# Kernel tuning notes

Hardware: AMD Instinct MI355X
Metric: run time of the kernel (lower is better)

## Reference

```python
import jax, jax.numpy as jnp
import numpy as np

B, T, D, H = 2, 2048, 1024, 16
HD = D // H  # head dim = 64


def setup_inputs() -> dict:
    key = jax.random.key(0)
    ks = jax.random.split(key, 8)
    scale = 0.02
    return {
        "query_states": jax.random.normal(ks[0], (B, T, D), jnp.float32),
        "key_states": jax.random.normal(ks[1], (B, T, D), jnp.float32),
        "query_mask": jnp.ones((B, T), jnp.float32),
        "key_mask": jnp.ones((B, T), jnp.float32),
        "Wq": jax.random.normal(ks[2], (D, D), jnp.float32) * scale,
        "bq": jnp.zeros((D,), jnp.float32),
        "Wk": jax.random.normal(ks[3], (D, D), jnp.float32) * scale,
        "bk": jnp.zeros((D,), jnp.float32),
        "Wv": jax.random.normal(ks[4], (D, D), jnp.float32) * scale,
        "bv": jnp.zeros((D,), jnp.float32),
        "mask_future": 1,
    }


def _split_heads(x):  # [B,T,D] -> [B,H,T,HD]
    return x.reshape(B, T, H, HD).transpose(0, 2, 1, 3)


def reference(query_states, key_states, query_mask, key_mask, Wq, bq, Wk, bk, Wv, bv, mask_future):
    q = _split_heads(query_states @ Wq.T + bq)
    k = _split_heads(key_states @ Wk.T + bk)
    v = _split_heads(key_states @ Wv.T + bv)
    # [B,H,T,T]
    scores = jnp.einsum("bhqd,bhkd->bhqk", q, k) / jnp.sqrt(jnp.float32(HD))
    scores = scores + (1.0 - key_mask)[:, None, None, :] * -10000.0
    if mask_future:
        causal = (1.0 - jnp.tril(jnp.ones((T, T), jnp.float32))) * -10000.0
        scores = scores + causal[None, None, :, :]
    probs = jax.nn.softmax(scores, axis=-1)
    probs = probs * query_mask[:, None, :, None]  # post-softmax query mask
    ctx = jnp.einsum("bhqk,bhkd->bhqd", probs, v)
    return ctx.transpose(0, 2, 1, 3).reshape(B, T, D)
```

## Files before the change

### kernel.cpp

```cpp
#include <hip/hip_runtime.h>
#include <hip/hip_bf16.h>
#include <stdint.h>

typedef __attribute__((ext_vector_type(8))) short short8;
typedef __attribute__((ext_vector_type(4))) short short4_t;
typedef __attribute__((ext_vector_type(4))) float f32x4;

#define B_ 2
#define T_ 2048
#define D_ 1024
#define H_ 16
#define HD_ 64
#define BT_ 4096
#define NKT64 32

#define QSCALE 0.1803368801111601f
#define PEN2 14426.950408889634f

__device__ __forceinline__ unsigned short f2bf(float f) {
    union { float f; uint32_t u; } v; v.f = f;
    uint32_t u = v.u;
    uint32_t r = (u + 0x7fffu + ((u >> 16) & 1u)) >> 16;
    return (unsigned short)r;
}

__device__ __forceinline__ uint32_t cvtpk(float a, float b) {
    union { __hip_bfloat162 h; uint32_t u; } cv;
    cv.h = __float22bfloat162_rn(make_float2(a, b));
    return cv.u;
}

__device__ __forceinline__ void gld16(const void* g, void* l) {
    __builtin_amdgcn_global_load_lds((const __attribute__((address_space(1))) void*)g,
                                     (__attribute__((address_space(3))) void*)l, 16, 0, 0);
}

__device__ __forceinline__ int swz(int x) { return x ^ (((x >> 7) & 7) << 4); }

__global__ __launch_bounds__(256) void cvt_all(const float* __restrict__ xq, unsigned short* __restrict__ dxq,
                                               const float* __restrict__ xk, unsigned short* __restrict__ dxk,
                                               const float* __restrict__ Wq, unsigned short* __restrict__ dwq,
                                               const float* __restrict__ Wk, unsigned short* __restrict__ dwk,
                                               const float* __restrict__ Wv, unsigned short* __restrict__ dwv,
                                               const float* __restrict__ kmask, float* __restrict__ kpen_g) {
    const int NX = BT_ * D_ / 8;
    const int NW = D_ * D_ / 8;
    const int NKP = B_ * T_ / 8;
    const int total = NX * 2 + NW * 3 + NKP;
    for (int i = blockIdx.x * 256 + threadIdx.x; i < total; i += gridDim.x * 256) {
        int j = i;
        const float* s;
        unsigned short* d;
        if (j < NX) { s = xq; d = dxq; }
        else if ((j -= NX) < NX) { s = xk; d = dxk; }
        else if ((j -= NX) < NW) { s = Wq; d = dwq; }
        else if ((j -= NW) < NW) { s = Wk; d = dwk; }
        else if ((j -= NW) < NW) { s = Wv; d = dwv; }
        else {
            j -= NW;
            const float4* mk = (const float4*)kmask + (size_t)j * 2;
            float4 a = mk[0], b4 = mk[1];
            float4 o0 = make_float4((1.0f - a.x) * -PEN2, (1.0f - a.y) * -PEN2,
                                    (1.0f - a.z) * -PEN2, (1.0f - a.w) * -PEN2);
            float4 o1 = make_float4((1.0f - b4.x) * -PEN2, (1.0f - b4.y) * -PEN2,
                                    (1.0f - b4.z) * -PEN2, (1.0f - b4.w) * -PEN2);
            ((float4*)kpen_g)[j * 2] = o0;
            ((float4*)kpen_g)[j * 2 + 1] = o1;
            continue;
        }
        const float4* sp = (const float4*)s + (size_t)j * 2;
        float4 a = sp[0], b4 = sp[1];
        short8 o;
        o[0] = (short)f2bf(a.x);  o[1] = (short)f2bf(a.y);
        o[2] = (short)f2bf(a.z);  o[3] = (short)f2bf(a.w);
        o[4] = (short)f2bf(b4.x); o[5] = (short)f2bf(b4.y);
        o[6] = (short)f2bf(b4.z); o[7] = (short)f2bf(b4.w);
        *(short8*)(d + (size_t)j * 8) = o;
    }
}

__global__ __launch_bounds__(256) void qkv_gemm_fused(const unsigned short* __restrict__ xq,
                                                      const unsigned short* __restrict__ xk,
                                                      const unsigned short* __restrict__ wq,
                                                      const unsigned short* __restrict__ wk,
                                                      const unsigned short* __restrict__ wv,
                                                      const float* __restrict__ bq,
                                                      const float* __restrict__ bk,
                                                      const float* __restrict__ bv,
                                                      unsigned short* __restrict__ q_ws,
                                                      unsigned short* __restrict__ k_ws,
                                                      unsigned short* __restrict__ v8_ws) {
    __shared__ unsigned short Al[128 * 32];
    __shared__ unsigned short Bl[128 * 32];
    const int K = D_;
    int z = blockIdx.z;
    const unsigned short* X = (z == 0) ? xq : xk;
    const unsigned short* W = (z == 0) ? wq : (z == 1 ? wk : wv);
    const float* bias = (z == 0) ? bq : (z == 1 ? bk : bv);

    int m0 = blockIdx.x * 128, n0 = blockIdx.y * 128;
    int tid = threadIdx.x, lane = tid & 63, w = tid >> 6;
    int wr = w >> 1, wc = w & 1;

    f32x4 acc[4][4];
#pragma unroll
    for (int i = 0; i < 4; i++)
#pragma unroll
        for (int j = 0; j < 4; j++) acc[i][j] = (f32x4){0.f, 0.f, 0.f, 0.f};

    int srow0 = (lane >> 2);
    int skch = (lane & 3) * 8;

    for (int kt = 0; kt < K / 32; ++kt) {
        int kb = kt * 32;
#pragma unroll
        for (int t = 0; t < 2; ++t) {
            int ins = w * 2 + t;
            int row = ins * 16 + srow0;
            gld16(X + (size_t)(m0 + row) * K + kb + skch, (char*)Al + ins * 1024);
            gld16(W + (size_t)(n0 + row) * K + kb + skch, (char*)Bl + ins * 1024);
        }
        __syncthreads();
        short8 af[4], bf[4];
#pragma unroll
        for (int mi = 0; mi < 4; mi++)
            af[mi] = *(const short8*)(Al + (wr * 64 + mi * 16 + (lane & 15)) * 32 + (lane >> 4) * 8);
#pragma unroll
        for (int ni = 0; ni < 4; ni++)
            bf[ni] = *(const short8*)(Bl + (wc * 64 + ni * 16 + (lane & 15)) * 32 + (lane >> 4) * 8);
#pragma unroll
        for (int mi = 0; mi < 4; mi++)
#pragma unroll
            for (int ni = 0; ni < 4; ni++)
                acc[mi][ni] = __builtin_amdgcn_mfma_f32_16x16x32_bf16(af[mi], bf[ni], acc[mi][ni], 0, 0, 0);
        __syncthreads();
    }

    if (z < 2) {
        unsigned short* outp = (z == 0) ? q_ws : k_ws;
        float osc = (z == 0) ? QSCALE : 1.0f;
#pragma unroll
        for (int ni = 0; ni < 4; ni++) {
            int n = n0 + wc * 64 + ni * 16 + (lane & 15);
            float bv2 = bias[n];
            int h = n >> 6, hd = n & 63;
#pragma unroll
            for (int mi = 0; mi < 4; mi++) {
#pragma unroll
                for (int r = 0; r < 4; r++) {
                    int m = m0 + wr * 64 + mi * 16 + (lane >> 4) * 4 + r;
                    int b = m >> 11, t = m & (T_ - 1);
                    outp[((size_t)(b * H_ + h) * T_ + t) * HD_ + hd] = f2bf((acc[mi][ni][r] + bv2) * osc);
                }
            }
        }
    } else {
#pragma unroll
        for (int ni = 0; ni < 4; ni++) {
            int n = n0 + wc * 64 + ni * 16 + (lane & 15);
            float bv2 = bias[n];
            int h = n >> 6, hd = n & 63;
#pragma unroll
            for (int mi = 0; mi < 4; mi++) {
                int m = m0 + wr * 64 + mi * 16 + (lane >> 4) * 4;
                int b = m >> 11, t = m & (T_ - 1);
                short4_t pk;
#pragma unroll
                for (int r = 0; r < 4; r++) pk[r] = (short)f2bf(acc[mi][ni][r] + bv2);
                *(short4_t*)(v8_ws + (((size_t)(b * H_ + h) * 256 + (t >> 3)) * HD_ + hd) * 8 + (t & 7)) = pk;
            }
        }
    }
}

__global__ __launch_bounds__(128) void attn(const unsigned short* __restrict__ q_ws,
                                            const unsigned short* __restrict__ k_ws,
                                            const unsigned short* __restrict__ v8_ws,
                                            const float* __restrict__ qmask,
                                            const float* __restrict__ kpen_g,
                                            const int* __restrict__ mfp,
                                            float* __restrict__ out) {
    __shared__ char SH[16384 + 512];

    int w = threadIdx.x >> 6;
    int lane = threadIdx.x & 63;
    int lg = lane >> 4, q = lane & 15;
    int bid = blockIdx.x;
    int qt = 63 - (bid >> 5);
    int bh = bid & 31;
    int b = bh >> 4, h = bh & 15;
    int q0 = qt * 32;
    int mf = mfp[0];
    int nkt = mf ? (qt >> 1) + 1 : NKT64;
    char* Pw = SH + w * 4096;

    short8 qf[2][2];
#pragma unroll
    for (int m = 0; m < 2; m++) {
        const unsigned short* qp = q_ws + ((size_t)bh * T_ + q0 + m * 16 + q) * HD_ + lg * 8;
        qf[m][0] = *(const short8*)qp;
        qf[m][1] = *(const short8*)(qp + 32);
    }

    f32x4 o[2][4];
#pragma unroll
    for (int m = 0; m < 2; m++)
#pragma unroll
        for (int i = 0; i < 4; i++) o[m][i] = (f32x4){0.f, 0.f, 0.f, 0.f};
    float lrow[2] = {0.f, 0.f};

    const float* kpenb = kpen_g + b * T_;

    for (int kt = w; kt < nkt; kt += 2) {
        int kv0 = kt * 64;

        f32x4 s[2][4];
        __builtin_amdgcn_s_setprio(1);
#pragma unroll
        for (int nb = 0; nb < 4; nb++) {
            const unsigned short* kp = k_ws + ((size_t)bh * T_ + kv0 + nb * 16 + q) * HD_ + lg * 8;
            short8 kf0 = *(const short8*)kp;
            short8 kf1 = *(const short8*)(kp + 32);
#pragma unroll
            for (int m = 0; m < 2; m++) {
                f32x4 z = (f32x4){0.f, 0.f, 0.f, 0.f};
                z = __builtin_amdgcn_mfma_f32_16x16x32_bf16(kf0, qf[m][0], z, 0, 0, 0);
                z = __builtin_amdgcn_mfma_f32_16x16x32_bf16(kf1, qf[m][1], z, 0, 0, 0);
                s[m][nb] = z;
            }
        }
        __builtin_amdgcn_s_setprio(0);

        short8 vf[4][2];
        const unsigned short* vbase = v8_ws + (((size_t)bh * 256 + (kv0 >> 3) + lg) * 64 + q) * 8;
#pragma unroll
        for (int nbh = 0; nbh < 4; nbh++) {
            vf[nbh][0] = *(const short8*)(vbase + nbh * 128);
            vf[nbh][1] = *(const short8*)(vbase + nbh * 128 + 2048);
        }

        f32x4 kp4[4];
#pragma unroll
        for (int nb = 0; nb < 4; nb++)
            kp4[nb] = *(const f32x4*)(kpenb + kv0 + nb * 16 + lg * 4);

        bool diag = mf && (kv0 + 63 > q0);
#pragma unroll
        for (int m = 0; m < 2; m++) {
            int qg = q0 + m * 16 + q;
#pragma unroll
            for (int nb = 0; nb < 4; nb++) {
#pragma unroll
                for (int r = 0; r < 4; r++) {
                    float v = s[m][nb][r] + kp4[nb][r];
                    if (diag) {
                        int kvg = kv0 + nb * 16 + lg * 4 + r;
                        v = (kvg > qg) ? v - PEN2 : v;
                    }
                    s[m][nb][r] = __builtin_amdgcn_exp2f(v);
                }
            }
            float rs = ((s[m][0][0] + s[m][0][1]) + (s[m][0][2] + s[m][0][3]))
                     + ((s[m][1][0] + s[m][1][1]) + (s[m][1][2] + s[m][1][3]))
                     + ((s[m][2][0] + s[m][2][1]) + (s[m][2][2] + s[m][2][3]))
                     + ((s[m][3][0] + s[m][3][1]) + (s[m][3][2] + s[m][3][3]));
            lrow[m] += rs;

#pragma unroll
            for (int nb = 0; nb < 4; nb++) {
                uint2 ww;
                ww.x = cvtpk(s[m][nb][0], s[m][nb][1]);
                ww.y = cvtpk(s[m][nb][2], s[m][nb][3]);
                *(uint2*)(Pw + m * 2048 + swz(q * 128 + nb * 32 + lg * 8)) = ww;
            }
        }

        short8 pf[2][2];
#pragma unroll
        for (int m = 0; m < 2; m++) {
            pf[m][0] = *(const short8*)(Pw + m * 2048 + swz(q * 128 + lg * 16));
            pf[m][1] = *(const short8*)(Pw + m * 2048 + swz(q * 128 + 64 + lg * 16));
        }

        __builtin_amdgcn_s_setprio(1);
#pragma unroll
        for (int nbh = 0; nbh < 4; nbh++) {
#pragma unroll
            for (int m = 0; m < 2; m++) {
                o[m][nbh] = __builtin_amdgcn_mfma_f32_16x16x32_bf16(vf[nbh][0], pf[m][0], o[m][nbh], 0, 0, 0);
                o[m][nbh] = __builtin_amdgcn_mfma_f32_16x16x32_bf16(vf[nbh][1], pf[m][1], o[m][nbh], 0, 0, 0);
            }
        }
        __builtin_amdgcn_s_setprio(0);
    }

#pragma unroll
    for (int m = 0; m < 2; m++) {
        lrow[m] += __shfl_xor(lrow[m], 16);
        lrow[m] += __shfl_xor(lrow[m], 32);
    }

    __syncthreads();
    float* OS = (float*)SH;
    float* ML = (float*)(SH + 16384);
#pragma unroll
    for (int m = 0; m < 2; m++)
#pragma unroll
        for (int nbh = 0; nbh < 4; nbh++)
            *(f32x4*)(OS + w * 2048 + ((m * 4 + nbh) * 64 + lane) * 4) = o[m][nbh];
    if (lane < 16) {
#pragma unroll
        for (int m = 0; m < 2; m++)
            ML[(w * 2 + m) * 16 + q] = lrow[m];
    }
    __syncthreads();

    {
        int m = w;
        float den = ML[(0 * 2 + m) * 16 + q] + ML[(1 * 2 + m) * 16 + q];
        int qg = q0 + m * 16 + q;
        float inv = qmask[b * T_ + qg] / den;
        float* op = out + ((size_t)(b * T_ + qg)) * D_ + h * 64 + lg * 4;
#pragma unroll
        for (int nbh = 0; nbh < 4; nbh++) {
            f32x4 OA = *(const f32x4*)(OS + 0 * 2048 + ((m * 4 + nbh) * 64 + lane) * 4);
            f32x4 OB = *(const f32x4*)(OS + 1 * 2048 + ((m * 4 + nbh) * 64 + lane) * 4);
            f32x4 ov;
#pragma unroll
            for (int r = 0; r < 4; r++)
                ov[r] = (OA[r] + OB[r]) * inv;
            *(f32x4*)(op + nbh * 16) = ov;
        }
    }
}

extern "C" void kernel_launch(void* const* d_in, const int* in_sizes, int n_in,
                              void* d_out, int out_size, void* d_ws, size_t ws_size,
                              hipStream_t stream) {
    const float* xq = (const float*)d_in[0];
    const float* xk = (const float*)d_in[1];
    const float* qmask = (const float*)d_in[2];
    const float* kmask = (const float*)d_in[3];
    const float* Wq = (const float*)d_in[4];
    const float* bq = (const float*)d_in[5];
    const float* Wk = (const float*)d_in[6];
    const float* bk = (const float*)d_in[7];
    const float* Wv = (const float*)d_in[8];
    const float* bv = (const float*)d_in[9];
    const int* mf = (const int*)d_in[10];
    float* out = (float*)d_out;

    char* ws = (char*)d_ws;
    unsigned short* xq_bf = (unsigned short*)(ws);
    unsigned short* xk_bf = (unsigned short*)(ws + (8u << 20));
    unsigned short* wq_bf = (unsigned short*)(ws + (16u << 20));
    unsigned short* wk_bf = (unsigned short*)(ws + (18u << 20));
    unsigned short* wv_bf = (unsigned short*)(ws + (20u << 20));
    unsigned short* q_ws  = (unsigned short*)(ws + (22u << 20));
    unsigned short* k_ws  = (unsigned short*)(ws + (30u << 20));
    unsigned short* v8_ws = (unsigned short*)(ws + (38u << 20));
    float* kpen_g         = (float*)(ws + (46u << 20));

    cvt_all<<<2048, 256, 0, stream>>>(xq, xq_bf, xk, xk_bf, Wq, wq_bf, Wk, wk_bf, Wv, wv_bf,
                                      kmask, kpen_g);

    dim3 gg(BT_ / 128, D_ / 128, 3);
    qkv_gemm_fused<<<gg, 256, 0, stream>>>(xq_bf, xk_bf, wq_bf, wk_bf, wv_bf, bq, bk, bv,
                                           q_ws, k_ws, v8_ws);

    attn<<<2048, 128, 0, stream>>>(q_ws, k_ws, v8_ws, qmask, kpen_g, mf, out);
}
```

Baseline: 112.4 us.

## Halve attention query tile to 16 rows and double grid size

Each attention block now handles 16 query rows instead of 32, so the grid doubles to 4096 blocks and registers and LDS per block shrink. The goal is more parallelism and occupancy, plus finer causal load balancing on the diagonal. The cost is that each K/V tile loaded from global memory is reused by only 16 query rows, which doubles K/V traffic and lowers MFMA work per load.

Result: slower. 151.7 us (+35.0%).

```diff
diff --git a/kernel.cpp b/kernel.cpp
--- a/kernel.cpp
+++ b/kernel.cpp
@@ -180,54 +180,46 @@
                                             const float* __restrict__ kpen_g,
                                             const int* __restrict__ mfp,
                                             float* __restrict__ out) {
-    __shared__ char SH[16384 + 512];
+    __shared__ char SH[8192 + 128];
 
     int w = threadIdx.x >> 6;
     int lane = threadIdx.x & 63;
     int lg = lane >> 4, q = lane & 15;
     int bid = blockIdx.x;
-    int qt = 63 - (bid >> 5);
+    int qt = 127 - (bid >> 5);
     int bh = bid & 31;
     int b = bh >> 4, h = bh & 15;
-    int q0 = qt * 32;
+    int q0 = qt * 16;
+    int qg = q0 + q;
     int mf = mfp[0];
-    int nkt = mf ? (qt >> 1) + 1 : NKT64;
-    char* Pw = SH + w * 4096;
-
-    short8 qf[2][2];
-#pragma unroll
-    for (int m = 0; m < 2; m++) {
-        const unsigned short* qp = q_ws + ((size_t)bh * T_ + q0 + m * 16 + q) * HD_ + lg * 8;
-        qf[m][0] = *(const short8*)qp;
-        qf[m][1] = *(const short8*)(qp + 32);
-    }
-
-    f32x4 o[2][4];
-#pragma unroll
-    for (int m = 0; m < 2; m++)
-#pragma unroll
-        for (int i = 0; i < 4; i++) o[m][i] = (f32x4){0.f, 0.f, 0.f, 0.f};
-    float lrow[2] = {0.f, 0.f};
+    int nkt = mf ? (qt >> 2) + 1 : NKT64;
+    char* Pw = SH + w * 2048;
+
+    const unsigned short* qp = q_ws + ((size_t)bh * T_ + qg) * HD_ + lg * 8;
+    short8 qf0 = *(const short8*)qp;
+    short8 qf1 = *(const short8*)(qp + 32);
+
+    f32x4 o[4];
+#pragma unroll
+    for (int i = 0; i < 4; i++) o[i] = (f32x4){0.f, 0.f, 0.f, 0.f};
+    float lrow = 0.f;
 
     const float* kpenb = kpen_g + b * T_;
 
     for (int kt = w; kt < nkt; kt += 2) {
         int kv0 = kt * 64;
 
-        f32x4 s[2][4];
+        f32x4 s[4];
         __builtin_amdgcn_s_setprio(1);
 #pragma unroll
         for (int nb = 0; nb < 4; nb++) {
             const unsigned short* kp = k_ws + ((size_t)bh * T_ + kv0 + nb * 16 + q) * HD_ + lg * 8;
             short8 kf0 = *(const short8*)kp;
             short8 kf1 = *(const short8*)(kp + 32);
-#pragma unroll
-            for (int m = 0; m < 2; m++) {
-                f32x4 z = (f32x4){0.f, 0.f, 0.f, 0.f};
-                z = __builtin_amdgcn_mfma_f32_16x16x32_bf16(kf0, qf[m][0], z, 0, 0, 0);
-                z = __builtin_amdgcn_mfma_f32_16x16x32_bf16(kf1, qf[m][1], z, 0, 0, 0);
-                s[m][nb] = z;
-            }
+            f32x4 z = (f32x4){0.f, 0.f, 0.f, 0.f};
+            z = __builtin_amdgcn_mfma_f32_16x16x32_bf16(kf0, qf0, z, 0, 0, 0);
+            z = __builtin_amdgcn_mfma_f32_16x16x32_bf16(kf1, qf1, z, 0, 0, 0);
+            s[nb] = z;
         }
         __builtin_amdgcn_s_setprio(0);
 
@@ -246,85 +238,61 @@
 
         bool diag = mf && (kv0 + 63 > q0);
 #pragma unroll
-        for (int m = 0; m < 2; m++) {
-            int qg = q0 + m * 16 + q;
-#pragma unroll
-            for (int nb = 0; nb < 4; nb++) {
-#pragma unroll
-                for (int r = 0; r < 4; r++) {
-                    float v = s[m][nb][r] + kp4[nb][r];
-                    if (diag) {
-                        int kvg = kv0 + nb * 16 + lg * 4 + r;
-                        v = (kvg > qg) ? v - PEN2 : v;
-                    }
-                    s[m][nb][r] = __builtin_amdgcn_exp2f(v);
+        for (int nb = 0; nb < 4; nb++) {
+#pragma unroll
+            for (int r = 0; r < 4; r++) {
+                float v = s[nb][r] + kp4[nb][r];
+                if (diag) {
+                    int kvg = kv0 + nb * 16 + lg * 4 + r;
+                    v = (kvg > qg) ? v - PEN2 : v;
                 }
+                s[nb][r] = __builtin_amdgcn_exp2f(v);
             }
-            float rs = ((s[m][0][0] + s[m][0][1]) + (s[m][0][2] + s[m][0][3]))
-                     + ((s[m][1][0] + s[m][1][1]) + (s[m][1][2] + s[m][1][3]))
-                     + ((s[m][2][0] + s[m][2][1]) + (s[m][2][2] + s[m][2][3]))
-                     + ((s[m][3][0] + s[m][3][1]) + (s[m][3][2] + s[m][3][3]));
-            lrow[m] += rs;
-
-#pragma unroll
-            for (int nb = 0; nb < 4; nb++) {
-                uint2 ww;
-                ww.x = cvtpk(s[m][nb][0], s[m][nb][1]);
-                ww.y = cvtpk(s[m][nb][2], s[m][nb][3]);
-                *(uint2*)(Pw + m * 2048 + swz(q * 128 + nb * 32 + lg * 8)) = ww;
-            }
-        }
-
-        short8 pf[2][2];
-#pragma unroll
-        for (int m = 0; m < 2; m++) {
-            pf[m][0] = *(const short8*)(Pw + m * 2048 + swz(q * 128 + lg * 16));
-            pf[m][1] = *(const short8*)(Pw + m * 2048 + swz(q * 128 + 64 + lg * 16));
-        }
+        }
+        lrow += ((s[0][0] + s[0][1]) + (s[0][2] + s[0][3])) + ((s[1][0] + s[1][1]) + (s[1][2] + s[1][3]))
+              + ((s[2][0] + s[2][1]) + (s[2][2] + s[2][3])) + ((s[3][0] + s[3][1]) + (s[3][2] + s[3][3]));
+
+#pragma unroll
+        for (int nb = 0; nb < 4; nb++) {
+            uint2 ww;
+            ww.x = cvtpk(s[nb][0], s[nb][1]);
+            ww.y = cvtpk(s[nb][2], s[nb][3]);
+            *(uint2*)(Pw + swz(q * 128 + nb * 32 + lg * 8)) = ww;
+        }
+
+        short8 pf0 = *(const short8*)(Pw + swz(q * 128 + lg * 16));
+        short8 pf1 = *(const short8*)(Pw + swz(q * 128 + 64 + lg * 16));
 
         __builtin_amdgcn_s_setprio(1);
 #pragma unroll
         for (int nbh = 0; nbh < 4; nbh++) {
-#pragma unroll
-            for (int m = 0; m < 2; m++) {
-                o[m][nbh] = __builtin_amdgcn_mfma_f32_16x16x32_bf16(vf[nbh][0], pf[m][0], o[m][nbh], 0, 0, 0);
-                o[m][nbh] = __builtin_amdgcn_mfma_f32_16x16x32_bf16(vf[nbh][1], pf[m][1], o[m][nbh], 0, 0, 0);
-            }
+            o[nbh] = __builtin_amdgcn_mfma_f32_16x16x32_bf16(vf[nbh][0], pf0, o[nbh], 0, 0, 0);
+            o[nbh] = __builtin_amdgcn_mfma_f32_16x16x32_bf16(vf[nbh][1], pf1, o[nbh], 0, 0, 0);
         }
         __builtin_amdgcn_s_setprio(0);
     }
 
-#pragma unroll
-    for (int m = 0; m < 2; m++) {
-        lrow[m] += __shfl_xor(lrow[m], 16);
-        lrow[m] += __shfl_xor(lrow[m], 32);
-    }
+    lrow += __shfl_xor(lrow, 16);
+    lrow += __shfl_xor(lrow, 32);
 
     __syncthreads();
     float* OS = (float*)SH;
-    float* ML = (float*)(SH + 16384);
-#pragma unroll
-    for (int m = 0; m < 2; m++)
-#pragma unroll
-        for (int nbh = 0; nbh < 4; nbh++)
-            *(f32x4*)(OS + w * 2048 + ((m * 4 + nbh) * 64 + lane) * 4) = o[m][nbh];
-    if (lane < 16) {
-#pragma unroll
-        for (int m = 0; m < 2; m++)
-            ML[(w * 2 + m) * 16 + q] = lrow[m];
-    }
+    float* ML = (float*)(SH + 8192);
+#pragma unroll
+    for (int nbh = 0; nbh < 4; nbh++)
+        *(f32x4*)(OS + ((w * 4 + nbh) * 64 + lane) * 4) = o[nbh];
+    if (lane < 16) ML[w * 16 + q] = lrow;
     __syncthreads();
 
     {
-        int m = w;
-        float den = ML[(0 * 2 + m) * 16 + q] + ML[(1 * 2 + m) * 16 + q];
-        int qg = q0 + m * 16 + q;
+        float den = ML[q] + ML[16 + q];
         float inv = qmask[b * T_ + qg] / den;
         float* op = out + ((size_t)(b * T_ + qg)) * D_ + h * 64 + lg * 4;
 #pragma unroll
-        for (int nbh = 0; nbh < 4; nbh++) {
-            f32x4 OA = *(const f32x4*)(OS + 0 * 2048 + ((m * 4 + nbh) * 64 + lane) * 4);
-            f32x4 OB = *(const f32x4*)(OS + 1 * 2048 + ((m * 4 + nbh) * 64 + lane) * 4);
+        for (int j = 0; j < 2; j++) {
+            int nbh = w * 2 + j;
+            f32x4 OA = *(const f32x4*)(OS + ((0 * 4 + nbh) * 64 + lane) * 4);
+            f32x4 OB = *(const f32x4*)(OS + ((1 * 4 + nbh) * 64 + lane) * 4);
             f32x4 ov;
 #pragma unroll
             for (int r = 0; r < 4; r++)
@@ -368,5 +336,5 @@
     qkv_gemm_fused<<<gg, 256, 0, stream>>>(xq_bf, xk_bf, wq_bf, wk_bf, wv_bf, bq, bk, bv,
                                            q_ws, k_ws, v8_ws);
 
-    attn<<<2048, 128, 0, stream>>>(q_ws, k_ws, v8_ws, qmask, kpen_g, mf, out);
-}
+    attn<<<4096, 128, 0, stream>>>(q_ws, k_ws, v8_ws, qmask, kpen_g, mf, out);
+}
```
